# Optimization experiments

Hardware: AMD Instinct MI355X
Metric: run time of the kernel (lower is better)

Reference implementation:

```python
import jax, jax.numpy as jnp
import numpy as np

N_NODES = 100000
N_EDGES = 1600000
D_IN = 128
HIDDEN = 128
D_OUT = 40
EPS = 1e-12  # F.normalize eps


def _glorot(key, shape):
    lim = float(np.sqrt(6.0 / (shape[0] + shape[1])))
    return jax.random.uniform(key, shape, jnp.float32, -lim, lim)


def setup_inputs() -> dict:
    key = jax.random.key(0)
    ks = jax.random.split(key, 8)
    x = jax.random.normal(ks[0], (N_NODES, D_IN), jnp.float32)
    edge_index = jax.random.randint(ks[1], (2, N_EDGES), 0, N_NODES, jnp.int64)
    return {
        "x": x,
        "edge_index": edge_index,
        "W_l1": _glorot(ks[2], (D_IN, HIDDEN)),
        "b_l1": jnp.zeros((HIDDEN,), jnp.float32),
        "W_r1": _glorot(ks[3], (D_IN, HIDDEN)),
        "W_l2": _glorot(ks[4], (HIDDEN, D_OUT)),
        "b_l2": jnp.zeros((D_OUT,), jnp.float32),
        "W_r2": _glorot(ks[5], (HIDDEN, D_OUT)),
    }


def _sage_conv(x, src, dst, W_l, b_l, W_r):
    # mean aggregation of source-node features into destination nodes
    n = x.shape[0]
    summed = jax.ops.segment_sum(x[src], dst, num_segments=n)          # [N, d]
    deg = jax.ops.segment_sum(jnp.ones_like(dst, x.dtype), dst, num_segments=n)
    mean = summed / jnp.maximum(deg, 1.0)[:, None]
    out = mean @ W_l + b_l + x @ W_r                                   # [N, d_out]
    # normalize=True: L2 row-normalize
    norm = jnp.maximum(jnp.linalg.norm(out, axis=-1, keepdims=True), EPS)
    return out / norm


def reference(x, edge_index, W_l1, b_l1, W_r1, W_l2, b_l2, W_r2):
    src, dst = edge_index[0], edge_index[1]
    # dropout p=0.6 is identity at inference (training=False)
    h = jax.nn.relu(_sage_conv(x, src, dst, W_l1, b_l1, W_r1))
    out = _sage_conv(h, src, dst, W_l2, b_l2, W_r2)
    return jax.nn.log_softmax(out, axis=1)
```

## Files before the change

### kernel.cpp

```cpp
#include <hip/hip_runtime.h>
#include <math.h>

#define N_NODES 100000
#define N_EDGES 1600000
#define D_IN 128
#define HIDDEN 128
#define D_OUT 40
#define EPSN 1e-12f

#define NBUCK 391
#define EPB 4096
#define NPART ((N_EDGES + EPB - 1) / EPB)
#define PEPB 16384
#define PNPART ((N_EDGES + PEPB - 1) / PEPB)

#define SWZ1_TOTAL (8 * 8 * 4 * 16 * 8)
#define SWZ2_TOTAL (4 * 8 * 4 * 16 * 8)
#define CASTB ((N_NODES * 16) / 256)
#define SWZB ((SWZ1_TOTAL + SWZ2_TOTAL + 255) / 256)

typedef __attribute__((ext_vector_type(8))) short short8;
typedef __attribute__((ext_vector_type(4))) float float4v;
typedef __attribute__((ext_vector_type(2))) float float2v;

static __device__ inline unsigned short f2bf(float f) {
    union { float f; unsigned u; } v; v.f = f;
    unsigned r = v.u + 0x7fffu + ((v.u >> 16) & 1u);
    return (unsigned short)(r >> 16);
}
static __device__ inline float bflo(unsigned u) {
    union { unsigned u; float f; } v; v.u = u << 16;
    return v.f;
}
static __device__ inline float bfhi(unsigned u) {
    union { unsigned u; float f; } v; v.u = u & 0xffff0000u;
    return v.f;
}

#if defined(__has_builtin)
#if __has_builtin(__builtin_amdgcn_cvt_pk_f32_fp8) && __has_builtin(__builtin_amdgcn_cvt_pk_fp8_f32)
#define HAVE_HW_FP8 1
#endif
#endif

static __device__ inline float2v fp8lo(unsigned u) {
#ifdef HAVE_HW_FP8
    return __builtin_amdgcn_cvt_pk_f32_fp8(u, false);
#else
    unsigned b0 = u & 0xffu, b1 = (u >> 8) & 0xffu;
    union { unsigned u; float f; } v0, v1;
    v0.u = ((b0 & 0x80u) << 24) | ((b0 & 0x7fu) << 20);
    v1.u = ((b1 & 0x80u) << 24) | ((b1 & 0x7fu) << 20);
    float2v r; r.x = v0.f * 0x1p+120f; r.y = v1.f * 0x1p+120f;
    return r;
#endif
}
static __device__ inline float2v fp8hi(unsigned u) {
#ifdef HAVE_HW_FP8
    return __builtin_amdgcn_cvt_pk_f32_fp8(u, true);
#else
    unsigned b0 = (u >> 16) & 0xffu, b1 = (u >> 24) & 0xffu;
    union { unsigned u; float f; } v0, v1;
    v0.u = ((b0 & 0x80u) << 24) | ((b0 & 0x7fu) << 20);
    v1.u = ((b1 & 0x80u) << 24) | ((b1 & 0x7fu) << 20);
    float2v r; r.x = v0.f * 0x1p+120f; r.y = v1.f * 0x1p+120f;
    return r;
#endif
}
#ifndef HAVE_HW_FP8
static __device__ inline unsigned enc1(float x) {
    union { float f; unsigned u; } v; v.f = x * 0x1p-120f;
    unsigned um = v.u & 0x7fffffffu;
    unsigned r = um + 0x7FFFFu + ((um >> 20) & 1u);
    return ((r >> 20) & 0x7fu) | ((v.u >> 24) & 0x80u);
}
#endif
static __device__ inline unsigned fp8pack(float f0, float f1, float f2, float f3) {
#ifdef HAVE_HW_FP8
    unsigned u = __builtin_amdgcn_cvt_pk_fp8_f32(f0, f1, 0u, false);
    u = __builtin_amdgcn_cvt_pk_fp8_f32(f2, f3, u, true);
    return u;
#else
    return enc1(f0) | (enc1(f1) << 8) | (enc1(f2) << 16) | (enc1(f3) << 24);
#endif
}

__global__ void prep_kernel(const int* __restrict__ dst, int* __restrict__ bucketCount,
                            const float* __restrict__ x, unsigned* __restrict__ xb,
                            unsigned* __restrict__ xf8,
                            const float* __restrict__ Wl1, const float* __restrict__ Wr1,
                            const float* __restrict__ Wl2, const float* __restrict__ Wr2,
                            unsigned short* __restrict__ out1, unsigned short* __restrict__ out2) {
    __shared__ int h[NBUCK];
    int b = blockIdx.x, t = threadIdx.x;
    if (b < NPART) {
        for (int i = t; i < NBUCK; i += 256) h[i] = 0;
        __syncthreads();
        int es = b * EPB;
        int ee = min(es + EPB, N_EDGES);
        for (int i = es + t; i < ee; i += 256) atomicAdd(&h[dst[i] >> 8], 1);
        __syncthreads();
        for (int i = t; i < NBUCK; i += 256)
            if (h[i]) atomicAdd(&bucketCount[i], h[i]);
        return;
    }
    b -= NPART;
    if (b < CASTB) {
        int g = b * 256 + t;
        const float4* x4 = (const float4*)x;
        float4 lo = x4[2 * g], hi = x4[2 * g + 1];
        uint4 o;
        o.x = (unsigned)f2bf(lo.x) | ((unsigned)f2bf(lo.y) << 16);
        o.y = (unsigned)f2bf(lo.z) | ((unsigned)f2bf(lo.w) << 16);
        o.z = (unsigned)f2bf(hi.x) | ((unsigned)f2bf(hi.y) << 16);
        o.w = (unsigned)f2bf(hi.z) | ((unsigned)f2bf(hi.w) << 16);
        ((uint4*)xb)[g] = o;
        uint2 o8;
        o8.x = fp8pack(lo.x, lo.y, lo.z, lo.w);
        o8.y = fp8pack(hi.x, hi.y, hi.z, hi.w);
        ((uint2*)xf8)[g] = o8;
        return;
    }
    b -= CASTB;
    {
        int idx = b * 256 + t;
        if (idx < SWZ1_TOTAL) {
            int j = idx & 7, l15 = (idx >> 3) & 15, quad = (idx >> 7) & 3;
            int rem = idx >> 9;
            int c = rem & 7, kt = rem >> 3;
            int k = kt * 32 + quad * 8 + j;
            int n = c * 16 + l15;
            float val = (k < 128) ? Wl1[k * HIDDEN + n] : Wr1[(k - 128) * HIDDEN + n];
            out1[idx] = f2bf(val);
        } else if (idx < SWZ1_TOTAL + SWZ2_TOTAL) {
            idx -= SWZ1_TOTAL;
            int j = idx & 7, l15 = (idx >> 3) & 15, quad = (idx >> 7) & 3;
            int rem = idx >> 9;
            int c = rem & 7, kt = rem >> 3;
            int k = kt * 32 + quad * 8 + j;
            int n = c * 16 + l15;
            float val = 0.0f;
            if (n < D_OUT) val = Wl2[k * D_OUT + n];
            else if (n >= 64 && n < 64 + D_OUT) val = Wr2[k * D_OUT + (n - 64)];
            out2[idx] = f2bf(val);
        }
    }
}

__global__ void bscan_kernel(const int* __restrict__ bc, int* __restrict__ bstart,
                             int* __restrict__ cursor) {
    __shared__ int s[256];
    int t = threadIdx.x;
    int a = (2 * t < NBUCK) ? bc[2 * t] : 0;
    int b = (2 * t + 1 < NBUCK) ? bc[2 * t + 1] : 0;
    int tp = a + b;
    s[t] = tp;
    __syncthreads();
    for (int off = 1; off < 256; off <<= 1) {
        int tmp = (t >= off) ? s[t - off] : 0;
        __syncthreads();
        s[t] += tmp;
        __syncthreads();
    }
    int texcl = s[t] - tp;
    if (2 * t < NBUCK) { bstart[2 * t] = texcl; cursor[2 * t] = texcl; }
    if (2 * t + 1 < NBUCK) { bstart[2 * t + 1] = texcl + a; cursor[2 * t + 1] = texcl + a; }
    if (t == 255) bstart[NBUCK] = s[255];
}

__global__ __launch_bounds__(512) void bpart_kernel(
    const int* __restrict__ src, const int* __restrict__ dst,
    int* __restrict__ cursor, unsigned* __restrict__ pairs) {
    __shared__ int h[NBUCK];
    __shared__ int base[NBUCK];
    int t = threadIdx.x;
    for (int i = t; i < NBUCK; i += 512) h[i] = 0;
    __syncthreads();
    int es = blockIdx.x * PEPB;
    int ee = min(es + PEPB, N_EDGES);
    for (int i = es + t; i < ee; i += 512) atomicAdd(&h[dst[i] >> 8], 1);
    __syncthreads();
    for (int i = t; i < NBUCK; i += 512) {
        int c = h[i];
        base[i] = c ? atomicAdd(&cursor[i], c) : 0;
    }
    __syncthreads();
    for (int i = t; i < NBUCK; i += 512) h[i] = 0;
    __syncthreads();
    for (int i = es + t; i < ee; i += 512) {
        int d = dst[i];
        int bk = d >> 8;
        int r = atomicAdd(&h[bk], 1);
        pairs[base[bk] + r] = ((unsigned)src[i] << 8) | (unsigned)(d & 255);
    }
}

__global__ void csr_kernel(const unsigned* __restrict__ pairs, const int* __restrict__ bstart,
                           int* __restrict__ hist, int* __restrict__ rowStart,
                           int* __restrict__ sortedSrc) {
    __shared__ int cnt[256];
    __shared__ int sc[256];
    __shared__ int cur[256];
    int b = blockIdx.x, t = threadIdx.x;
    int es = bstart[b], ee = bstart[b + 1];
    cnt[t] = 0;
    __syncthreads();
    for (int i = es + t; i < ee; i += 256) atomicAdd(&cnt[pairs[i] & 255], 1);
    __syncthreads();
    int v = cnt[t];
    sc[t] = v;
    __syncthreads();
    for (int off = 1; off < 256; off <<= 1) {
        int tmp = (t >= off) ? sc[t - off] : 0;
        __syncthreads();
        sc[t] += tmp;
        __syncthreads();
    }
    int excl = sc[t] - v;
    int node = (b << 8) + t;
    if (node < N_NODES) {
        hist[node] = v;
        rowStart[node] = es + excl;
    }
    cur[t] = excl;
    __syncthreads();
    for (int i = es + t; i < ee; i += 256) {
        unsigned p = pairs[i];
        int r = atomicAdd(&cur[p & 255], 1);
        sortedSrc[es + r] = (int)(p >> 8);
    }
}

#define ACC2(v)                                                                   \
    { a[0] += fp8lo(v.x); a[1] += fp8hi(v.x);                                     \
      a[2] += fp8lo(v.y); a[3] += fp8hi(v.y); }

__global__ void agg_kernel(const uint2* __restrict__ xf8,
                           const int* __restrict__ sortedSrc,
                           const int* __restrict__ rowStart, const int* __restrict__ hist,
                           uint4* __restrict__ meanb) {
    int w = __builtin_amdgcn_readfirstlane((int)(threadIdx.x >> 6));
    int node = blockIdx.x * 4 + w;
    int lane = threadIdx.x & 63;
    int g = lane >> 4, sl = lane & 15;
    int s0 = __builtin_amdgcn_readfirstlane(rowStart[node]);
    int cnt = __builtin_amdgcn_readfirstlane(hist[node]);
    float2v a[4];
#pragma unroll
    for (int e = 0; e < 4; e++) a[e] = (float2v){0.f, 0.f};
    int i = 0;
    for (; i + 16 <= cnt; i += 16) {
        int sA = sortedSrc[s0 + i + g];
        int sB = sortedSrc[s0 + i + 4 + g];
        int sC = sortedSrc[s0 + i + 8 + g];
        int sD = sortedSrc[s0 + i + 12 + g];
        uint2 vA = xf8[sA * 16 + sl];
        uint2 vB = xf8[sB * 16 + sl];
        uint2 vC = xf8[sC * 16 + sl];
        uint2 vD = xf8[sD * 16 + sl];
        ACC2(vA)
        ACC2(vB)
        ACC2(vC)
        ACC2(vD)
    }
    for (; i + 4 <= cnt; i += 4) {
        int s = sortedSrc[s0 + i + g];
        uint2 v = xf8[s * 16 + sl];
        ACC2(v)
    }
    if (g < cnt - i) {
        int s = sortedSrc[s0 + i + g];
        uint2 v = xf8[s * 16 + sl];
        ACC2(v)
    }
#pragma unroll
    for (int e = 0; e < 4; e++) {
        a[e].x += __shfl_xor(a[e].x, 16, 64);
        a[e].y += __shfl_xor(a[e].y, 16, 64);
    }
#pragma unroll
    for (int e = 0; e < 4; e++) {
        a[e].x += __shfl_xor(a[e].x, 32, 64);
        a[e].y += __shfl_xor(a[e].y, 32, 64);
    }
    if (g == 0) {
        float dinv = 1.0f / fmaxf((float)cnt, 1.0f);
        uint4 o;
        o.x = (unsigned)f2bf(a[0].x * dinv) | ((unsigned)f2bf(a[0].y * dinv) << 16);
        o.y = (unsigned)f2bf(a[1].x * dinv) | ((unsigned)f2bf(a[1].y * dinv) << 16);
        o.z = (unsigned)f2bf(a[2].x * dinv) | ((unsigned)f2bf(a[2].y * dinv) << 16);
        o.w = (unsigned)f2bf(a[3].x * dinv) | ((unsigned)f2bf(a[3].y * dinv) << 16);
        meanb[node * 16 + sl] = o;
    }
}

__global__ __launch_bounds__(256) void gemm1g_kernel(
    const unsigned short* __restrict__ meanb, const unsigned short* __restrict__ xb,
    const short* __restrict__ bswz1, const float* __restrict__ bias1,
    const short* __restrict__ bswz2,
    unsigned short* __restrict__ g_l, unsigned short* __restrict__ g_r) {
    __shared__ unsigned short hT[4][16][140];
    int tid = threadIdx.x;
    int w = __builtin_amdgcn_readfirstlane(tid >> 6);
    int lane = tid & 63;
    int l15 = lane & 15, quad = lane >> 4;
    int n0 = blockIdx.x * 64;
    int nodeA = n0 + w * 16 + l15;
    if (nodeA >= N_NODES) nodeA = N_NODES - 1;

    float4v acc[8];
#pragma unroll
    for (int c = 0; c < 8; c++) acc[c] = (float4v){0.f, 0.f, 0.f, 0.f};
#pragma unroll
    for (int kt = 0; kt < 8; kt++) {
        const unsigned short* ab = (kt < 4) ? meanb : xb;
        short8 a = *(const short8*)(ab + (size_t)nodeA * 128 + (kt & 3) * 32 + quad * 8);
#pragma unroll
        for (int c = 0; c < 8; c++) {
            short8 b = *(const short8*)(bswz1 + (((kt * 8 + c) * 4 + quad) * 16 + l15) * 8);
            acc[c] = __builtin_amdgcn_mfma_f32_16x16x32_bf16(a, b, acc[c], 0, 0, 0);
        }
    }

    float v[8][4];
    float ss[4] = {0.f, 0.f, 0.f, 0.f};
#pragma unroll
    for (int c = 0; c < 8; c++) {
        float bi = bias1[c * 16 + l15];
#pragma unroll
        for (int r = 0; r < 4; r++) {
            float t = acc[c][r] + bi;
            v[c][r] = t;
            ss[r] += t * t;
        }
    }
#pragma unroll
    for (int r = 0; r < 4; r++)
        for (int off = 1; off < 16; off <<= 1) ss[r] += __shfl_xor(ss[r], off, 64);
#pragma unroll
    for (int r = 0; r < 4; r++) {
        float inv = 1.0f / fmaxf(sqrtf(ss[r]), EPSN);
#pragma unroll
        for (int c = 0; c < 8; c++) {
            hT[w][quad * 4 + r][c * 16 + l15] = f2bf(fmaxf(v[c][r] * inv, 0.0f));
        }
    }

    float4v acc2[8];
#pragma unroll
    for (int c = 0; c < 8; c++) acc2[c] = (float4v){0.f, 0.f, 0.f, 0.f};
#pragma unroll
    for (int kt = 0; kt < 4; kt++) {
        short8 a = *(const short8*)&hT[w][l15][kt * 32 + quad * 8];
#pragma unroll
        for (int c = 0; c < 8; c++) {
            short8 b = *(const short8*)(bswz2 + (((kt * 8 + c) * 4 + quad) * 16 + l15) * 8);
            acc2[c] = __builtin_amdgcn_mfma_f32_16x16x32_bf16(a, b, acc2[c], 0, 0, 0);
        }
    }
#pragma unroll
    for (int r = 0; r < 4; r++) {
        int node = n0 + w * 16 + quad * 4 + r;
        if (node < N_NODES) {
#pragma unroll
            for (int c = 0; c < 4; c++)
                g_l[(size_t)node * 64 + c * 16 + l15] = f2bf(acc2[c][r]);
#pragma unroll
            for (int c = 4; c < 8; c++)
                g_r[(size_t)node * 64 + (c - 4) * 16 + l15] = f2bf(acc2[c][r]);
        }
    }
}

#define ACCB(v)                                                                   \
    { A[0] += (float2v){bflo(v.x), bfhi(v.x)};                                    \
      A[1] += (float2v){bflo(v.y), bfhi(v.y)};                                    \
      A[2] += (float2v){bflo(v.z), bfhi(v.z)};                                    \
      A[3] += (float2v){bflo(v.w), bfhi(v.w)}; }

__global__ void fused2h_kernel(const uint4* __restrict__ g_l4, const uint4* __restrict__ g_r4,
                               const int* __restrict__ sortedSrc,
                               const int* __restrict__ rowStart, const int* __restrict__ hist,
                               const float* __restrict__ bias, float* __restrict__ out) {
    int tid = threadIdx.x;
    int w = __builtin_amdgcn_readfirstlane(tid >> 6);
    int lane = tid & 63;
    int g = lane >> 4, q1 = (lane >> 3) & 1, sl = lane & 7;
    int node = blockIdx.x * 16 + w * 4 + g;
    int s0 = rowStart[node];
    int cnt = hist[node];
    float2v A[4];
#pragma unroll
    for (int e = 0; e < 4; e++) A[e] = (float2v){0.f, 0.f};
    int i = 0;
    for (; i + 8 <= cnt; i += 8) {
        int sA = sortedSrc[s0 + i + q1];
        int sB = sortedSrc[s0 + i + 2 + q1];
        int sC = sortedSrc[s0 + i + 4 + q1];
        int sD = sortedSrc[s0 + i + 6 + q1];
        uint4 vA = g_l4[(size_t)sA * 8 + sl];
        uint4 vB = g_l4[(size_t)sB * 8 + sl];
        uint4 vC = g_l4[(size_t)sC * 8 + sl];
        uint4 vD = g_l4[(size_t)sD * 8 + sl];
        ACCB(vA)
        ACCB(vB)
        ACCB(vC)
        ACCB(vD)
    }
    for (; i + 2 <= cnt; i += 2) {
        int s = sortedSrc[s0 + i + q1];
        uint4 v = g_l4[(size_t)s * 8 + sl];
        ACCB(v)
    }
    if (i + q1 < cnt) {
        int s = sortedSrc[s0 + i + q1];
        uint4 v = g_l4[(size_t)s * 8 + sl];
        ACCB(v)
    }
    float a0 = A[0].x, a1 = A[0].y, a2 = A[1].x, a3 = A[1].y;
    float a4 = A[2].x, a5 = A[2].y, a6 = A[3].x, a7 = A[3].y;
    a0 += __shfl_xor(a0, 8, 64);
    a1 += __shfl_xor(a1, 8, 64);
    a2 += __shfl_xor(a2, 8, 64);
    a3 += __shfl_xor(a3, 8, 64);
    a4 += __shfl_xor(a4, 8, 64);
    a5 += __shfl_xor(a5, 8, 64);
    a6 += __shfl_xor(a6, 8, 64);
    a7 += __shfl_xor(a7, 8, 64);
    float dinv = 1.0f / fmaxf((float)cnt, 1.0f);
    uint4 gr = g_r4[(size_t)node * 8 + sl];
    bool valid = (sl < 5);
    float b0 = 0, b1 = 0, b2 = 0, b3 = 0, b4 = 0, b5 = 0, b6 = 0, b7 = 0;
    if (valid) {
        b0 = bias[sl * 8 + 0]; b1 = bias[sl * 8 + 1]; b2 = bias[sl * 8 + 2]; b3 = bias[sl * 8 + 3];
        b4 = bias[sl * 8 + 4]; b5 = bias[sl * 8 + 5]; b6 = bias[sl * 8 + 6]; b7 = bias[sl * 8 + 7];
    }
    float t0 = a0 * dinv + bflo(gr.x) + b0;
    float t1 = a1 * dinv + bfhi(gr.x) + b1;
    float t2 = a2 * dinv + bflo(gr.y) + b2;
    float t3 = a3 * dinv + bfhi(gr.y) + b3;
    float t4 = a4 * dinv + bflo(gr.z) + b4;
    float t5 = a5 * dinv + bfhi(gr.z) + b5;
    float t6 = a6 * dinv + bflo(gr.w) + b6;
    float t7 = a7 * dinv + bfhi(gr.w) + b7;
    float ssq = t0 * t0 + t1 * t1 + t2 * t2 + t3 * t3 + t4 * t4 + t5 * t5 + t6 * t6 + t7 * t7;
    ssq += __shfl_xor(ssq, 1, 64); ssq += __shfl_xor(ssq, 2, 64); ssq += __shfl_xor(ssq, 4, 64);
    float inv = 1.0f / fmaxf(sqrtf(ssq), EPSN);
    float v0 = t0 * inv, v1 = t1 * inv, v2 = t2 * inv, v3 = t3 * inv;
    float v4 = t4 * inv, v5 = t5 * inv, v6 = t6 * inv, v7 = t7 * inv;
    float m = valid ? fmaxf(fmaxf(fmaxf(v0, v1), fmaxf(v2, v3)),
                            fmaxf(fmaxf(v4, v5), fmaxf(v6, v7))) : -INFINITY;
    m = fmaxf(m, __shfl_xor(m, 1, 64));
    m = fmaxf(m, __shfl_xor(m, 2, 64));
    m = fmaxf(m, __shfl_xor(m, 4, 64));
    float se = 0.0f;
    if (valid) {
        se = expf(v0 - m) + expf(v1 - m) + expf(v2 - m) + expf(v3 - m) +
             expf(v4 - m) + expf(v5 - m) + expf(v6 - m) + expf(v7 - m);
    }
    se += __shfl_xor(se, 1, 64); se += __shfl_xor(se, 2, 64); se += __shfl_xor(se, 4, 64);
    float ls = logf(se) + m;
    if (q1 == 0 && valid) {
        float* o = out + (size_t)node * D_OUT + sl * 8;
        ((float4*)o)[0] = (float4){v0 - ls, v1 - ls, v2 - ls, v3 - ls};
        ((float4*)o)[1] = (float4){v4 - ls, v5 - ls, v6 - ls, v7 - ls};
    }
}

static inline size_t align256(size_t x) { return (x + 255) & ~(size_t)255; }

extern "C" void kernel_launch(void* const* d_in, const int* in_sizes, int n_in,
                              void* d_out, int out_size, void* d_ws, size_t ws_size,
                              hipStream_t stream) {
    const float* x   = (const float*)d_in[0];
    const int*   ei  = (const int*)d_in[1];
    const float* Wl1 = (const float*)d_in[2];
    const float* bl1 = (const float*)d_in[3];
    const float* Wr1 = (const float*)d_in[4];
    const float* Wl2 = (const float*)d_in[5];
    const float* bl2 = (const float*)d_in[6];
    const float* Wr2 = (const float*)d_in[7];
    float* out = (float*)d_out;

    const int* src = ei;
    const int* dst = ei + N_EDGES;

    char* ws = (char*)d_ws;
    size_t off = 0;
    int* bucketCount = (int*)(ws + off); off += align256((size_t)NBUCK * 4);
    int* bucketStart = (int*)(ws + off); off += align256((size_t)(NBUCK + 1) * 4);
    int* cursor      = (int*)(ws + off); off += align256((size_t)NBUCK * 4);
    int* hist        = (int*)(ws + off); off += align256((size_t)N_NODES * 4);
    int* rowStart    = (int*)(ws + off); off += align256((size_t)N_NODES * 4);
    unsigned* pairs  = (unsigned*)(ws + off); off += align256((size_t)N_EDGES * 4);
    int* sortedSrc   = (int*)(ws + off); off += align256((size_t)N_EDGES * 4);
    unsigned* xb     = (unsigned*)(ws + off); off += align256((size_t)N_NODES * 128 * 2);
    unsigned* xf8    = (unsigned*)(ws + off); off += align256((size_t)N_NODES * 128);
    unsigned* meanb  = (unsigned*)(ws + off); off += align256((size_t)N_NODES * 128 * 2);
    unsigned short* g_l = (unsigned short*)(ws + off); off += align256((size_t)N_NODES * 64 * 2);
    unsigned short* g_r = (unsigned short*)(ws + off); off += align256((size_t)N_NODES * 64 * 2);
    unsigned short* bswz1 = (unsigned short*)(ws + off); off += align256((size_t)SWZ1_TOTAL * 2);
    unsigned short* bswz2 = (unsigned short*)(ws + off); off += align256((size_t)SWZ2_TOTAL * 2);

    hipMemsetAsync(bucketCount, 0, (size_t)NBUCK * 4, stream);

    prep_kernel<<<NPART + CASTB + SWZB, 256, 0, stream>>>(
        dst, bucketCount, x, xb, xf8, Wl1, Wr1, Wl2, Wr2, bswz1, bswz2);
    bscan_kernel<<<1, 256, 0, stream>>>(bucketCount, bucketStart, cursor);
    bpart_kernel<<<PNPART, 512, 0, stream>>>(src, dst, cursor, pairs);
    csr_kernel<<<NBUCK, 256, 0, stream>>>(pairs, bucketStart, hist, rowStart, sortedSrc);

    agg_kernel<<<N_NODES / 4, 256, 0, stream>>>((const uint2*)xf8, sortedSrc, rowStart, hist,
                                                (uint4*)meanb);
    gemm1g_kernel<<<(N_NODES + 63) / 64, 256, 0, stream>>>(
        (const unsigned short*)meanb, (const unsigned short*)xb,
        (const short*)bswz1, bl1, (const short*)bswz2, g_l, g_r);
    fused2h_kernel<<<N_NODES / 16, 256, 0, stream>>>(
        (const uint4*)g_l, (const uint4*)g_r, sortedSrc, rowStart, hist, bl2, out);
}
```

Measured before the change: 291.6 us.

## Replace two-level bucket CSR build with global atomic histogram, scan and scatter

Replaces the bucketed partition and per-bucket CSR construction with a per-node global atomic histogram, a three-pass prefix scan (block scan, block-sum scan, offset add), and a direct atomic-cursor scatter of source indices. This removes the intermediate pairs buffer and one full pass over edges through LDS, but relies on 1.6M global atomics, which land on random addresses, in both the counting and the scatter pass. The order of sources within each row becomes nondeterministic, so the aggregation order changes and memory locality of sortedSrc writes is worse.

```diff
diff --git a/kernel.cpp b/kernel.cpp
--- a/kernel.cpp
+++ b/kernel.cpp
@@ -11,8 +11,6 @@
 #define NBUCK 391
 #define EPB 4096
 #define NPART ((N_EDGES + EPB - 1) / EPB)
-#define PEPB 16384
-#define PNPART ((N_EDGES + PEPB - 1) / PEPB)
 
 #define SWZ1_TOTAL (8 * 8 * 4 * 16 * 8)
 #define SWZ2_TOTAL (4 * 8 * 4 * 16 * 8)
@@ -85,23 +83,17 @@
 #endif
 }
 
-__global__ void prep_kernel(const int* __restrict__ dst, int* __restrict__ bucketCount,
+__global__ void prep_kernel(const int* __restrict__ dst, int* __restrict__ hist,
                             const float* __restrict__ x, unsigned* __restrict__ xb,
                             unsigned* __restrict__ xf8,
                             const float* __restrict__ Wl1, const float* __restrict__ Wr1,
                             const float* __restrict__ Wl2, const float* __restrict__ Wr2,
                             unsigned short* __restrict__ out1, unsigned short* __restrict__ out2) {
-    __shared__ int h[NBUCK];
     int b = blockIdx.x, t = threadIdx.x;
     if (b < NPART) {
-        for (int i = t; i < NBUCK; i += 256) h[i] = 0;
-        __syncthreads();
         int es = b * EPB;
         int ee = min(es + EPB, N_EDGES);
-        for (int i = es + t; i < ee; i += 256) atomicAdd(&h[dst[i] >> 8], 1);
-        __syncthreads();
-        for (int i = t; i < NBUCK; i += 256)
-            if (h[i]) atomicAdd(&bucketCount[i], h[i]);
+        for (int i = es + t; i < ee; i += 256) atomicAdd(&hist[dst[i]], 1);
         return;
     }
     b -= NPART;
@@ -147,8 +139,25 @@
     }
 }
 
-__global__ void bscan_kernel(const int* __restrict__ bc, int* __restrict__ bstart,
-                             int* __restrict__ cursor) {
+__global__ void s1_kernel(const int* __restrict__ hist, int* __restrict__ rowStart,
+                          int* __restrict__ blockSum) {
+    __shared__ int s[256];
+    int b = blockIdx.x, t = threadIdx.x;
+    int node = b * 256 + t;
+    int v = (node < N_NODES) ? hist[node] : 0;
+    s[t] = v;
+    __syncthreads();
+    for (int off = 1; off < 256; off <<= 1) {
+        int tmp = (t >= off) ? s[t - off] : 0;
+        __syncthreads();
+        s[t] += tmp;
+        __syncthreads();
+    }
+    if (node < N_NODES) rowStart[node] = s[t] - v;
+    if (t == 255) blockSum[b] = s[255];
+}
+
+__global__ void bscan_kernel(const int* __restrict__ bc, int* __restrict__ bstart) {
     __shared__ int s[256];
     int t = threadIdx.x;
     int a = (2 * t < NBUCK) ? bc[2 * t] : 0;
@@ -163,71 +172,32 @@
         __syncthreads();
     }
     int texcl = s[t] - tp;
-    if (2 * t < NBUCK) { bstart[2 * t] = texcl; cursor[2 * t] = texcl; }
-    if (2 * t + 1 < NBUCK) { bstart[2 * t + 1] = texcl + a; cursor[2 * t + 1] = texcl + a; }
+    if (2 * t < NBUCK) bstart[2 * t] = texcl;
+    if (2 * t + 1 < NBUCK) bstart[2 * t + 1] = texcl + a;
     if (t == 255) bstart[NBUCK] = s[255];
 }
 
-__global__ __launch_bounds__(512) void bpart_kernel(
-    const int* __restrict__ src, const int* __restrict__ dst,
-    int* __restrict__ cursor, unsigned* __restrict__ pairs) {
-    __shared__ int h[NBUCK];
-    __shared__ int base[NBUCK];
-    int t = threadIdx.x;
-    for (int i = t; i < NBUCK; i += 512) h[i] = 0;
-    __syncthreads();
-    int es = blockIdx.x * PEPB;
-    int ee = min(es + PEPB, N_EDGES);
-    for (int i = es + t; i < ee; i += 512) atomicAdd(&h[dst[i] >> 8], 1);
-    __syncthreads();
-    for (int i = t; i < NBUCK; i += 512) {
-        int c = h[i];
-        base[i] = c ? atomicAdd(&cursor[i], c) : 0;
-    }
-    __syncthreads();
-    for (int i = t; i < NBUCK; i += 512) h[i] = 0;
-    __syncthreads();
-    for (int i = es + t; i < ee; i += 512) {
+__global__ void s3_kernel(int* __restrict__ rowStart, const int* __restrict__ blockOff,
+                          int* __restrict__ cursor) {
+    int b = blockIdx.x, t = threadIdx.x;
+    int node = b * 256 + t;
+    if (node < N_NODES) {
+        int v = rowStart[node] + blockOff[b];
+        rowStart[node] = v;
+        cursor[node] = v;
+    }
+}
+
+__global__ __launch_bounds__(256) void scatter_kernel(const int* __restrict__ src,
+                                                      const int* __restrict__ dst,
+                                                      int* __restrict__ cursor,
+                                                      int* __restrict__ sortedSrc) {
+    int es = blockIdx.x * EPB;
+    int ee = min(es + EPB, N_EDGES);
+    for (int i = es + threadIdx.x; i < ee; i += 256) {
         int d = dst[i];
-        int bk = d >> 8;
-        int r = atomicAdd(&h[bk], 1);
-        pairs[base[bk] + r] = ((unsigned)src[i] << 8) | (unsigned)(d & 255);
-    }
-}
-
-__global__ void csr_kernel(const unsigned* __restrict__ pairs, const int* __restrict__ bstart,
-                           int* __restrict__ hist, int* __restrict__ rowStart,
-                           int* __restrict__ sortedSrc) {
-    __shared__ int cnt[256];
-    __shared__ int sc[256];
-    __shared__ int cur[256];
-    int b = blockIdx.x, t = threadIdx.x;
-    int es = bstart[b], ee = bstart[b + 1];
-    cnt[t] = 0;
-    __syncthreads();
-    for (int i = es + t; i < ee; i += 256) atomicAdd(&cnt[pairs[i] & 255], 1);
-    __syncthreads();
-    int v = cnt[t];
-    sc[t] = v;
-    __syncthreads();
-    for (int off = 1; off < 256; off <<= 1) {
-        int tmp = (t >= off) ? sc[t - off] : 0;
-        __syncthreads();
-        sc[t] += tmp;
-        __syncthreads();
-    }
-    int excl = sc[t] - v;
-    int node = (b << 8) + t;
-    if (node < N_NODES) {
-        hist[node] = v;
-        rowStart[node] = es + excl;
-    }
-    cur[t] = excl;
-    __syncthreads();
-    for (int i = es + t; i < ee; i += 256) {
-        unsigned p = pairs[i];
-        int r = atomicAdd(&cur[p & 255], 1);
-        sortedSrc[es + r] = (int)(p >> 8);
+        int r = atomicAdd(&cursor[d], 1);
+        sortedSrc[r] = src[i];
     }
 }
 
@@ -487,12 +457,11 @@
 
     char* ws = (char*)d_ws;
     size_t off = 0;
-    int* bucketCount = (int*)(ws + off); off += align256((size_t)NBUCK * 4);
-    int* bucketStart = (int*)(ws + off); off += align256((size_t)(NBUCK + 1) * 4);
-    int* cursor      = (int*)(ws + off); off += align256((size_t)NBUCK * 4);
+    int* blockSum    = (int*)(ws + off); off += align256((size_t)NBUCK * 4);
+    int* blockOff    = (int*)(ws + off); off += align256((size_t)(NBUCK + 1) * 4);
+    int* cursor      = (int*)(ws + off); off += align256((size_t)N_NODES * 4);
     int* hist        = (int*)(ws + off); off += align256((size_t)N_NODES * 4);
     int* rowStart    = (int*)(ws + off); off += align256((size_t)N_NODES * 4);
-    unsigned* pairs  = (unsigned*)(ws + off); off += align256((size_t)N_EDGES * 4);
     int* sortedSrc   = (int*)(ws + off); off += align256((size_t)N_EDGES * 4);
     unsigned* xb     = (unsigned*)(ws + off); off += align256((size_t)N_NODES * 128 * 2);
     unsigned* xf8    = (unsigned*)(ws + off); off += align256((size_t)N_NODES * 128);
@@ -502,13 +471,14 @@
     unsigned short* bswz1 = (unsigned short*)(ws + off); off += align256((size_t)SWZ1_TOTAL * 2);
     unsigned short* bswz2 = (unsigned short*)(ws + off); off += align256((size_t)SWZ2_TOTAL * 2);
 
-    hipMemsetAsync(bucketCount, 0, (size_t)NBUCK * 4, stream);
+    hipMemsetAsync(hist, 0, (size_t)N_NODES * 4, stream);
 
     prep_kernel<<<NPART + CASTB + SWZB, 256, 0, stream>>>(
-        dst, bucketCount, x, xb, xf8, Wl1, Wr1, Wl2, Wr2, bswz1, bswz2);
-    bscan_kernel<<<1, 256, 0, stream>>>(bucketCount, bucketStart, cursor);
-    bpart_kernel<<<PNPART, 512, 0, stream>>>(src, dst, cursor, pairs);
-    csr_kernel<<<NBUCK, 256, 0, stream>>>(pairs, bucketStart, hist, rowStart, sortedSrc);
+        dst, hist, x, xb, xf8, Wl1, Wr1, Wl2, Wr2, bswz1, bswz2);
+    s1_kernel<<<NBUCK, 256, 0, stream>>>(hist, rowStart, blockSum);
+    bscan_kernel<<<1, 256, 0, stream>>>(blockSum, blockOff);
+    s3_kernel<<<NBUCK, 256, 0, stream>>>(rowStart, blockOff, cursor);
+    scatter_kernel<<<NPART, 256, 0, stream>>>(src, dst, cursor, sortedSrc);
 
     agg_kernel<<<N_NODES / 4, 256, 0, stream>>>((const uint2*)xf8, sortedSrc, rowStart, hist,
                                                 (uint4*)meanb);
```

After: 406.7 us. 39.5% more time.
